# Performance work log

Hardware: AMD Instinct MI355X
Metric: run time of the kernel (lower is better)

The kernel has to match this reference:

```python
import jax, jax.numpy as jnp
import numpy as np

N = 50000       # nodes
E = 800000      # edges
F_IN = 128      # dataset.num_node_features
H = 128         # hidden_channels (all equal), pool_dim
FC1, FC2 = 512, 256
G = 512         # number of graphs
C = 32          # dataset.num_classes
EPS = 1e-5      # BatchNorm eps


def setup_inputs() -> dict:
    key = jax.random.key(0)
    ks = jax.random.split(key, 16)
    rn = lambda k, s: jax.random.normal(k, s, jnp.float32) * 0.05
    return {
        "x": jax.random.normal(ks[0], (N, F_IN), jnp.float32),
        "edge_index": jax.random.randint(ks[1], (2, E), 0, N),
        "batch": jnp.sort(jax.random.randint(ks[2], (N,), 0, G)),
        "W1": rn(ks[3], (F_IN, H)), "b1": jnp.zeros((H,), jnp.float32),
        "W2": rn(ks[4], (H, H)),    "b2": jnp.zeros((H,), jnp.float32),
        "W3": rn(ks[5], (H, H)),    "b3": jnp.zeros((H,), jnp.float32),
        "W4": rn(ks[6], (H, H)),    "b4": jnp.zeros((H,), jnp.float32),
        "lw1": rn(ks[7], (H, FC1)),   "lb1": jnp.zeros((FC1,), jnp.float32),
        "lw2": rn(ks[8], (FC1, FC2)), "lb2": jnp.zeros((FC2,), jnp.float32),
        "lw3": rn(ks[9], (FC2, C)),   "lb3": jnp.zeros((C,), jnp.float32),
        "g1": jnp.ones((FC1,), jnp.float32), "be1": jnp.zeros((FC1,), jnp.float32),
        "g2": jnp.ones((FC2,), jnp.float32), "be2": jnp.zeros((FC2,), jnp.float32),
    }


def _gcn_structure(edge_index):
    # add self loops, then symmetric deg^-1/2 normalization (PyG GCNConv default)
    loop = jnp.arange(N)
    src = jnp.concatenate([edge_index[0], loop])
    dst = jnp.concatenate([edge_index[1], loop])
    deg = jax.ops.segment_sum(jnp.ones_like(src, jnp.float32), dst, num_segments=N)
    dinv = jnp.where(deg > 0, jax.lax.rsqrt(deg), 0.0)
    norm = dinv[src] * dinv[dst]          # [E + N]
    return src, dst, norm


def _gcn_conv(x, src, dst, norm, W, b):
    h = x @ W                              # [N, out]
    agg = jax.ops.segment_sum(h[src] * norm[:, None], dst, num_segments=N)
    return agg + b


def _bn(h, gamma, beta):
    # training-mode batch stats (biased variance), as torch BatchNorm1d
    m = jnp.mean(h, axis=0)
    v = jnp.var(h, axis=0)
    return (h - m) * jax.lax.rsqrt(v + EPS) * gamma + beta


def reference(x, edge_index, batch, W1, b1, W2, b2, W3, b3, W4, b4,
              lw1, lb1, lw2, lb2, lw3, lb3, g1, be1, g2, be2):
    src, dst, norm = _gcn_structure(edge_index)
    x = jax.nn.relu(_gcn_conv(x, src, dst, norm, W1, b1))
    x = jax.nn.relu(_gcn_conv(x, src, dst, norm, W2, b2))
    x = jax.nn.relu(_gcn_conv(x, src, dst, norm, W3, b3))
    x = jax.nn.relu(_gcn_conv(x, src, dst, norm, W4, b4))
    # global_add_pool over graphs
    p = jax.ops.segment_sum(x, batch, num_segments=G)   # [G, H]
    h = jax.nn.relu(p @ lw1 + lb1)
    h = _bn(h, g1, be1)                                  # dropout = identity (eval)
    h = jax.nn.relu(h @ lw2 + lb2)
    h = _bn(h, g2, be2)
    return jax.nn.sigmoid(h @ lw3 + lb3)                 # [G, C]
```

## Files before the change

kernel.cpp:

```cpp
#include <hip/hip_runtime.h>
#include <hip/hip_fp16.h>
#include <math.h>

#define NN 50000
#define NE 800000
#define FT 128
#define NG 512
#define F1 512
#define F2 256
#define NC 32
#define BN_EPS 1e-5f

typedef __attribute__((ext_vector_type(8))) unsigned short ushort8;
typedef __attribute__((ext_vector_type(8))) _Float16 f16x8;
typedef __attribute__((ext_vector_type(4))) float f32x4;

__device__ __forceinline__ unsigned short f2h(float f) {
  return __half_as_ushort(__float2half(f));
}
__device__ __forceinline__ float h2f(unsigned short h) {
  return __half2float(__ushort_as_half(h));
}


__global__ __launch_bounds__(256) void k_hist(const int* __restrict__ ei, int* __restrict__ cnt,
                                              unsigned short* __restrict__ rank16) {
  int e = blockIdx.x * 256 + threadIdx.x;
  if (e < NE) rank16[e] = (unsigned short)atomicAdd(&cnt[ei[NE + e]], 1);
}

__global__ __launch_bounds__(256) void k_dinv(const int* __restrict__ cnt, float* __restrict__ dinv) {
  int i = blockIdx.x * 256 + threadIdx.x;
  if (i < NN) dinv[i] = rsqrtf((float)(cnt[i] + 1));
}

__global__ __launch_bounds__(256) void k_scan1(const int* __restrict__ cnt, int* __restrict__ bsum) {
  __shared__ int s[256];
  int t = threadIdx.x, i = blockIdx.x * 256 + t;
  s[t] = (i < NN) ? cnt[i] : 0;
  __syncthreads();
  for (int d = 128; d > 0; d >>= 1) {
    if (t < d) s[t] += s[t + d];
    __syncthreads();
  }
  if (t == 0) bsum[blockIdx.x] = s[0];
}

__global__ __launch_bounds__(256) void k_scan2(const int* __restrict__ bsum, int* __restrict__ bscan, int nb) {
  __shared__ int s[256];
  int t = threadIdx.x;
  int v = (t < nb) ? bsum[t] : 0;
  s[t] = v; __syncthreads();
  for (int d = 1; d < 256; d <<= 1) {
    int a = (t >= d) ? s[t - d] : 0;
    __syncthreads();
    s[t] += a;
    __syncthreads();
  }
  bscan[t] = s[t] - v;
}

__global__ __launch_bounds__(256) void k_scan3(const int* __restrict__ cnt, const int* __restrict__ bscan,
                                               int* __restrict__ off) {
  __shared__ int s[256];
  int t = threadIdx.x, i = blockIdx.x * 256 + t;
  int v = (i < NN) ? cnt[i] : 0;
  s[t] = v; __syncthreads();
  for (int d = 1; d < 256; d <<= 1) {
    int a = (t >= d) ? s[t - d] : 0;
    __syncthreads();
    s[t] += a;
    __syncthreads();
  }
  int base = bscan[blockIdx.x];
  if (i < NN) off[i] = base + s[t] - v;
  if (i == NN - 1) off[NN] = base + s[t];
}

__global__ __launch_bounds__(256) void k_fill(const int* __restrict__ ei, const int* __restrict__ off,
                                              const unsigned short* __restrict__ rank16,
                                              const float* __restrict__ dinv,
                                              unsigned int* __restrict__ ep) {
  int e = blockIdx.x * 256 + threadIdx.x;
  if (e >= NE) return;
  int s = ei[e], d = ei[NE + e];
  int p = off[d] + (int)rank16[e];
  float w = dinv[s] * dinv[d];
  ep[p] = (unsigned int)(s & 0xFFFF) | ((unsigned int)f2h(w) << 16);
}


__global__ __launch_bounds__(256) void k_wprep4(const float* __restrict__ W0, const float* __restrict__ W1,
                                                const float* __restrict__ W2, const float* __restrict__ W3,
                                                unsigned short* __restrict__ Wt) {
  int idx = blockIdx.x * 256 + threadIdx.x;
  int l = idx >> 14;
  int r = idx & 16383;
  int c = r >> 7, k = r & 127;
  const float* W = (l == 0) ? W0 : (l == 1) ? W1 : (l == 2) ? W2 : W3;
  int byte = c * 256 + k * 2;
  byte ^= (c & 7) << 4;
  Wt[l * 16384 + (byte >> 1)] = f2h(W[k * FT + c]);
}


template <int FIRST>
__global__ __launch_bounds__(256) void k_gemm_mfma(const float* __restrict__ Xf,
                                                   const unsigned short* __restrict__ Xh,
                                                   const unsigned short* __restrict__ Wt,
                                                   unsigned short* __restrict__ Oc) {
  __shared__ unsigned short sA[64 * 128];
  __shared__ unsigned short sB[128 * 128];
  int t = threadIdx.x;
#pragma unroll
  for (int i = 0; i < 8; ++i) {
    int off = t * 16 + i * 4096;
    *(float4*)((char*)sB + off) = *(const float4*)((const char*)Wt + off);
  }
  {
    int row = t >> 2, k0 = (t & 3) * 32;
    int grow = blockIdx.x * 64 + row;
    if (grow >= NN) grow = NN - 1;
    if (FIRST) {
      const float* xr = Xf + (size_t)grow * FT + k0;
#pragma unroll
      for (int j = 0; j < 4; ++j) {
        float4 v0 = *(const float4*)&xr[j * 8];
        float4 v1 = *(const float4*)&xr[j * 8 + 4];
        ushort8 w;
        w[0] = f2h(v0.x); w[1] = f2h(v0.y); w[2] = f2h(v0.z); w[3] = f2h(v0.w);
        w[4] = f2h(v1.x); w[5] = f2h(v1.y); w[6] = f2h(v1.z); w[7] = f2h(v1.w);
        int byte = row * 256 + (k0 + j * 8) * 2;
        byte ^= (row & 7) << 4;
        *(ushort8*)((char*)sA + byte) = w;
      }
    } else {
#pragma unroll
      for (int j = 0; j < 4; ++j) {
        int k = k0 + j * 8;
        int ch = k >> 5, ko = k & 31;
        ushort8 v = *(const ushort8*)&Xh[((size_t)ch * NN + grow) * 32 + ko];
        int byte = row * 256 + k * 2;
        byte ^= (row & 7) << 4;
        *(ushort8*)((char*)sA + byte) = v;
      }
    }
  }
  __syncthreads();
  int w = t >> 6, l = t & 63;
  int m = l & 15, ks = l >> 4;
  f16x8 a[4];
#pragma unroll
  for (int kk = 0; kk < 4; ++kk) {
    int r = w * 16 + m;
    int byte = r * 256 + (kk * 32 + ks * 8) * 2;
    byte ^= (r & 7) << 4;
    a[kk] = *(const f16x8*)((const char*)sA + byte);
  }
  f32x4 acc[8];
#pragma unroll
  for (int nf = 0; nf < 8; ++nf) acc[nf] = (f32x4){0.f, 0.f, 0.f, 0.f};
#pragma unroll
  for (int nf = 0; nf < 8; ++nf) {
#pragma unroll
    for (int kk = 0; kk < 4; ++kk) {
      int col = nf * 16 + m;
      int byte = col * 256 + (kk * 32 + ks * 8) * 2;
      byte ^= (col & 7) << 4;
      f16x8 b = *(const f16x8*)((const char*)sB + byte);
      acc[nf] = __builtin_amdgcn_mfma_f32_16x16x32_f16(a[kk], b, acc[nf], 0, 0, 0);
    }
  }
  int orow0 = blockIdx.x * 64 + w * 16 + ks * 4;
#pragma unroll
  for (int nf = 0; nf < 8; ++nf) {
    int ch = nf >> 1;
    int co = ((nf & 1) << 4) + m;
#pragma unroll
    for (int r = 0; r < 4; ++r) {
      int orow = orow0 + r;
      if (orow < NN) Oc[((size_t)ch * NN + orow) * 32 + co] = f2h(acc[nf][r]);
    }
  }
}


__global__ __launch_bounds__(256) void k_aggc(const unsigned short* __restrict__ Hc,
                                              const float* __restrict__ dinv,
                                              const int* __restrict__ off, const unsigned int* __restrict__ ep,
                                              const float* __restrict__ bias, unsigned short* __restrict__ O) {
  int c = blockIdx.x & 3;
  int grp = blockIdx.x >> 2;
  int t = threadIdx.x;
  int node = grp * 64 + (t >> 2);
  int l = t & 3;
  if (node >= NN) return;
  const unsigned short* base = Hc + (size_t)c * NN * 32 + l * 8;
  float di = dinv[node];
  float sw = di * di;
  float acc[8];
  {
    ushort8 sv = *(const ushort8*)&base[(size_t)node * 32];
#pragma unroll
    for (int i = 0; i < 8; ++i) acc[i] = h2f(sv[i]) * sw;
  }
  int e0 = off[node], e1 = off[node + 1];
  int e = e0;
  for (; e + 8 <= e1; e += 8) {
    unsigned int pw[8];
#pragma unroll
    for (int j = 0; j < 8; ++j) pw[j] = ep[e + j];
    ushort8 v[8];
#pragma unroll
    for (int j = 0; j < 8; ++j) v[j] = *(const ushort8*)&base[(size_t)(pw[j] & 0xFFFFu) * 32];
#pragma unroll
    for (int j = 0; j < 8; ++j) {
      float w = h2f((unsigned short)(pw[j] >> 16));
#pragma unroll
      for (int i = 0; i < 8; ++i) acc[i] += h2f(v[j][i]) * w;
    }
  }
  for (; e + 4 <= e1; e += 4) {
    unsigned int p0 = ep[e], p1 = ep[e + 1], p2 = ep[e + 2], p3 = ep[e + 3];
    ushort8 v0 = *(const ushort8*)&base[(size_t)(p0 & 0xFFFFu) * 32];
    ushort8 v1 = *(const ushort8*)&base[(size_t)(p1 & 0xFFFFu) * 32];
    ushort8 v2 = *(const ushort8*)&base[(size_t)(p2 & 0xFFFFu) * 32];
    ushort8 v3 = *(const ushort8*)&base[(size_t)(p3 & 0xFFFFu) * 32];
    float w0 = h2f((unsigned short)(p0 >> 16));
    float w1 = h2f((unsigned short)(p1 >> 16));
    float w2 = h2f((unsigned short)(p2 >> 16));
    float w3 = h2f((unsigned short)(p3 >> 16));
#pragma unroll
    for (int i = 0; i < 8; ++i) acc[i] += h2f(v0[i]) * w0;
#pragma unroll
    for (int i = 0; i < 8; ++i) acc[i] += h2f(v1[i]) * w1;
#pragma unroll
    for (int i = 0; i < 8; ++i) acc[i] += h2f(v2[i]) * w2;
#pragma unroll
    for (int i = 0; i < 8; ++i) acc[i] += h2f(v3[i]) * w3;
  }
  for (; e < e1; ++e) {
    unsigned int pv = ep[e];
    float w = h2f((unsigned short)(pv >> 16));
    ushort8 v = *(const ushort8*)&base[(size_t)(pv & 0xFFFFu) * 32];
#pragma unroll
    for (int i = 0; i < 8; ++i) acc[i] += h2f(v[i]) * w;
  }
  ushort8 outv;
#pragma unroll
  for (int i = 0; i < 8; ++i) {
    float v = acc[i] + bias[c * 32 + l * 8 + i];
    outv[i] = f2h(fmaxf(v, 0.f));
  }
  *(ushort8*)&O[((size_t)c * NN + node) * 32 + l * 8] = outv;
}


__global__ __launch_bounds__(256) void k_bounds(const int* __restrict__ batch, int* __restrict__ gstart,
                                                int* __restrict__ gend) {
  int i = blockIdx.x * 256 + threadIdx.x;
  if (i >= NN) return;
  int b = batch[i];
  if (i == 0 || batch[i - 1] != b) gstart[b] = i;
  if (i == NN - 1 || batch[i + 1] != b) gend[b] = i + 1;
}

__global__ __launch_bounds__(128) void k_pool(const unsigned short* __restrict__ X, const int* __restrict__ gstart,
                                              const int* __restrict__ gend, float* __restrict__ pool) {
  int g = blockIdx.x, t = threadIdx.x;
  int ch = t >> 5, wo = t & 31;
  float s = 0.f;
  int n0 = gstart[g], n1 = gend[g];
  const unsigned short* base = X + (size_t)ch * NN * 32 + wo;
  for (int n = n0; n < n1; ++n) s += h2f(base[(size_t)n * 32]);
  pool[g * FT + t] = s;
}


__global__ __launch_bounds__(256) void k_fc1(const float* __restrict__ P, const float* __restrict__ W,
                                             const float* __restrict__ B, float* __restrict__ O) {
  __shared__ float sp[FT];
  int g = blockIdx.x, t = threadIdx.x;
  if (t < FT) sp[t] = P[g * FT + t];
  __syncthreads();
  float a0 = B[t], a1 = B[t + 256];
  for (int k = 0; k < FT; ++k) {
    float x = sp[k];
    a0 += x * W[k * F1 + t];
    a1 += x * W[k * F1 + t + 256];
  }
  O[g * F1 + t] = fmaxf(a0, 0.f);
  O[g * F1 + t + 256] = fmaxf(a1, 0.f);
}

__global__ __launch_bounds__(256) void k_bnstats(const float* __restrict__ h, int cols,
                                                 float* __restrict__ bm, float* __restrict__ br) {
  __shared__ float ss[256], s2[256];
  int c = blockIdx.x, t = threadIdx.x;
  float a = 0.f, b = 0.f;
  for (int r = t; r < NG; r += 256) {
    float v = h[r * cols + c];
    a += v; b += v * v;
  }
  ss[t] = a; s2[t] = b; __syncthreads();
  for (int d = 128; d > 0; d >>= 1) {
    if (t < d) { ss[t] += ss[t + d]; s2[t] += s2[t + d]; }
    __syncthreads();
  }
  if (t == 0) {
    float m = ss[0] / NG;
    float var = s2[0] / NG - m * m;
    bm[c] = m;
    br[c] = rsqrtf(var + BN_EPS);
  }
}

__global__ __launch_bounds__(256) void k_fc2(const float* __restrict__ H1, const float* __restrict__ bm,
                                             const float* __restrict__ br, const float* __restrict__ gam,
                                             const float* __restrict__ bet, const float* __restrict__ W,
                                             const float* __restrict__ B, float* __restrict__ O) {
  __shared__ float sh[F1];
  int g = blockIdx.x, t = threadIdx.x;
  for (int k = t; k < F1; k += 256) {
    float v = H1[g * F1 + k];
    sh[k] = (v - bm[k]) * br[k] * gam[k] + bet[k];
  }
  __syncthreads();
  float a = B[t];
  for (int k = 0; k < F1; ++k) a += sh[k] * W[k * F2 + t];
  O[g * F2 + t] = fmaxf(a, 0.f);
}

__global__ __launch_bounds__(256) void k_fc3(const float* __restrict__ H2, const float* __restrict__ bm,
                                             const float* __restrict__ br, const float* __restrict__ gam,
                                             const float* __restrict__ bet, const float* __restrict__ W,
                                             const float* __restrict__ B, float* __restrict__ O) {
  __shared__ float sh[F2];
  int g = blockIdx.x, t = threadIdx.x;
  if (t < F2) {
    float v = H2[g * F2 + t];
    sh[t] = (v - bm[t]) * br[t] * gam[t] + bet[t];
  }
  __syncthreads();
  if (t < NC) {
    float a = B[t];
    for (int k = 0; k < F2; ++k) a += sh[k] * W[k * NC + t];
    O[g * NC + t] = 1.f / (1.f + expf(-a));
  }
}


extern "C" void kernel_launch(void* const* d_in, const int* in_sizes, int n_in,
                              void* d_out, int out_size, void* d_ws, size_t ws_size,
                              hipStream_t stream) {
  const float* x     = (const float*)d_in[0];
  const int*   ei    = (const int*)d_in[1];
  const int*   batch = (const int*)d_in[2];
  const float* Wc[4] = {(const float*)d_in[3], (const float*)d_in[5], (const float*)d_in[7], (const float*)d_in[9]};
  const float* Bc[4] = {(const float*)d_in[4], (const float*)d_in[6], (const float*)d_in[8], (const float*)d_in[10]};
  const float* lw1 = (const float*)d_in[11]; const float* lb1 = (const float*)d_in[12];
  const float* lw2 = (const float*)d_in[13]; const float* lb2 = (const float*)d_in[14];
  const float* lw3 = (const float*)d_in[15]; const float* lb3 = (const float*)d_in[16];
  const float* g1  = (const float*)d_in[17]; const float* be1 = (const float*)d_in[18];
  const float* g2  = (const float*)d_in[19]; const float* be2 = (const float*)d_in[20];

  char* p = (char*)d_ws;
  auto take = [&](size_t bytes) {
    char* r = p;
    p += (bytes + 255) & ~(size_t)255;
    return r;
  };
  int*   cnt    = (int*)take((size_t)NN * 4);
  float* dinv   = (float*)take((size_t)NN * 4);
  int*   off    = (int*)take((size_t)(NN + 1) * 4);
  int*   bsum   = (int*)take(256 * 4);
  int*   bscan  = (int*)take(256 * 4);
  int*   gstart = (int*)take((size_t)NG * 4);
  int*   gend   = (int*)take((size_t)NG * 4);
  unsigned short* rank16 = (unsigned short*)take((size_t)NE * 2);
  unsigned int*   ep   = (unsigned int*)take((size_t)NE * 4);
  unsigned short* Wt   = (unsigned short*)take((size_t)4 * FT * FT * 2);
  unsigned short* bufT = (unsigned short*)take((size_t)NN * FT * 2);
  unsigned short* bufA = (unsigned short*)take((size_t)NN * FT * 2);
  unsigned short* bufB = (unsigned short*)take((size_t)NN * FT * 2);
  float* pool   = (float*)take((size_t)NG * FT * 4);
  float* h1     = (float*)take((size_t)NG * F1 * 4);
  float* h2     = (float*)take((size_t)NG * F2 * 4);
  float* bnm1   = (float*)take(F1 * 4);
  float* bnr1   = (float*)take(F1 * 4);
  float* bnm2   = (float*)take(F2 * 4);
  float* bnr2   = (float*)take(F2 * 4);

  const int NB = (NN + 255) / 256;

  hipMemsetAsync(cnt, 0, (size_t)NN * 4, stream);
  hipMemsetAsync(gstart, 0, (size_t)NG * 4, stream);
  hipMemsetAsync(gend, 0, (size_t)NG * 4, stream);

  k_hist<<<NE / 256, 256, 0, stream>>>(ei, cnt, rank16);
  k_dinv<<<NB, 256, 0, stream>>>(cnt, dinv);
  k_scan1<<<NB, 256, 0, stream>>>(cnt, bsum);
  k_scan2<<<1, 256, 0, stream>>>(bsum, bscan, NB);
  k_scan3<<<NB, 256, 0, stream>>>(cnt, bscan, off);
  k_fill<<<NE / 256, 256, 0, stream>>>(ei, off, rank16, dinv, ep);
  k_wprep4<<<256, 256, 0, stream>>>(Wc[0], Wc[1], Wc[2], Wc[3], Wt);

  const int NBLK_G = (NN + 63) / 64;
  const int NGRP_A = (NN + 63) / 64;
  unsigned short* outs[4] = {bufA, bufB, bufA, bufB};
  for (int l = 0; l < 4; ++l) {
    if (l == 0)
      k_gemm_mfma<1><<<NBLK_G, 256, 0, stream>>>(x, (const unsigned short*)nullptr, Wt, bufT);
    else
      k_gemm_mfma<0><<<NBLK_G, 256, 0, stream>>>((const float*)nullptr, outs[l - 1], Wt + (size_t)l * FT * FT, bufT);
    k_aggc<<<NGRP_A * 4, 256, 0, stream>>>(bufT, dinv, off, ep, Bc[l], outs[l]);
  }

  k_bounds<<<NB, 256, 0, stream>>>(batch, gstart, gend);
  k_pool<<<NG, 128, 0, stream>>>(bufB, gstart, gend, pool);

  k_fc1<<<NG, 256, 0, stream>>>(pool, lw1, lb1, h1);
  k_bnstats<<<F1, 256, 0, stream>>>(h1, F1, bnm1, bnr1);
  k_fc2<<<NG, 256, 0, stream>>>(h1, bnm1, bnr1, g1, be1, lw2, lb2, h2);
  k_bnstats<<<F2, 256, 0, stream>>>(h2, F2, bnm2, bnr2);
  k_fc3<<<NG, 256, 0, stream>>>(h2, bnm2, bnr2, g2, be2, lw3, lb3, (float*)d_out);
}
```

Before: 314.3 us.

## Privatize degree histogram into 8 copies and slice CSR fill by destination range

The degree histogram now uses 8 private count arrays, chosen by block index, to cut atomic contention, and each thread loads 8 edges with vector reads. A new k_sum kernel turns the per-copy counts into exclusive prefixes and writes the total degrees. k_fill runs 8 blocks per edge strip, each writing only edges whose destination falls in one slice of nodes, which is meant to localise the scattered writes to ep. This adds an extra kernel, a larger memset, and 8x redundant edge reads in the fill step.

```diff
diff --git a/kernel.cpp b/kernel.cpp
--- a/kernel.cpp
+++ b/kernel.cpp
@@ -10,6 +10,8 @@
 #define F2 256
 #define NC 32
 #define BN_EPS 1e-5f
+#define NSLC (NN / 8)
+#define NSTRIP ((NE + 2047) / 2048)
 
 typedef __attribute__((ext_vector_type(8))) unsigned short ushort8;
 typedef __attribute__((ext_vector_type(8))) _Float16 f16x8;
@@ -23,10 +25,33 @@
 }
 
 
-__global__ __launch_bounds__(256) void k_hist(const int* __restrict__ ei, int* __restrict__ cnt,
+__global__ __launch_bounds__(256) void k_hist(const int* __restrict__ ei, int* __restrict__ cnt8,
                                               unsigned short* __restrict__ rank16) {
-  int e = blockIdx.x * 256 + threadIdx.x;
-  if (e < NE) rank16[e] = (unsigned short)atomicAdd(&cnt[ei[NE + e]], 1);
+  int c = blockIdx.x & 7;
+  int e0 = blockIdx.x * 2048 + threadIdx.x * 8;
+  if (e0 >= NE) return;
+  int* cn = cnt8 + (size_t)c * NN;
+  const int* dst = ei + NE;
+  int4 a = *(const int4*)&dst[e0];
+  int4 b4 = *(const int4*)&dst[e0 + 4];
+  int d[8] = {a.x, a.y, a.z, a.w, b4.x, b4.y, b4.z, b4.w};
+  ushort8 r;
+#pragma unroll
+  for (int j = 0; j < 8; ++j) r[j] = (unsigned short)atomicAdd(&cn[d[j]], 1);
+  *(ushort8*)&rank16[e0] = r;
+}
+
+__global__ __launch_bounds__(256) void k_sum(int* __restrict__ cnt8, int* __restrict__ cnt) {
+  int n = blockIdx.x * 256 + threadIdx.x;
+  if (n >= NN) return;
+  int s = 0;
+#pragma unroll
+  for (int c = 0; c < 8; ++c) {
+    int v = cnt8[(size_t)c * NN + n];
+    cnt8[(size_t)c * NN + n] = s;
+    s += v;
+  }
+  cnt[n] = s;
 }
 
 __global__ __launch_bounds__(256) void k_dinv(const int* __restrict__ cnt, float* __restrict__ dinv) {
@@ -78,15 +103,32 @@
 }
 
 __global__ __launch_bounds__(256) void k_fill(const int* __restrict__ ei, const int* __restrict__ off,
+                                              const int* __restrict__ pre8,
                                               const unsigned short* __restrict__ rank16,
                                               const float* __restrict__ dinv,
                                               unsigned int* __restrict__ ep) {
-  int e = blockIdx.x * 256 + threadIdx.x;
-  if (e >= NE) return;
-  int s = ei[e], d = ei[NE + e];
-  int p = off[d] + (int)rank16[e];
-  float w = dinv[s] * dinv[d];
-  ep[p] = (unsigned int)(s & 0xFFFF) | ((unsigned int)f2h(w) << 16);
+  int c = blockIdx.x & 7;
+  int lo = c * NSLC, hi = lo + NSLC;
+  int strip = blockIdx.x >> 3;
+  int e0 = strip * 2048 + threadIdx.x * 8;
+  if (e0 >= NE) return;
+  const int* prec = pre8 + (size_t)(strip & 7) * NN;
+  const int* dst = ei + NE;
+  int4 da = *(const int4*)&dst[e0];
+  int4 db = *(const int4*)&dst[e0 + 4];
+  int4 sa = *(const int4*)&ei[e0];
+  int4 sb = *(const int4*)&ei[e0 + 4];
+  ushort8 rr = *(const ushort8*)&rank16[e0];
+  int d[8] = {da.x, da.y, da.z, da.w, db.x, db.y, db.z, db.w};
+  int s[8] = {sa.x, sa.y, sa.z, sa.w, sb.x, sb.y, sb.z, sb.w};
+#pragma unroll
+  for (int j = 0; j < 8; ++j) {
+    if (d[j] >= lo && d[j] < hi) {
+      int p = off[d[j]] + prec[d[j]] + (int)rr[j];
+      float w = dinv[s[j]] * dinv[d[j]];
+      ep[p] = (unsigned int)(s[j] & 0xFFFF) | ((unsigned int)f2h(w) << 16);
+    }
+  }
 }
 
 
@@ -370,6 +412,7 @@
     p += (bytes + 255) & ~(size_t)255;
     return r;
   };
+  int*   cnt8   = (int*)take((size_t)8 * NN * 4);
   int*   cnt    = (int*)take((size_t)NN * 4);
   float* dinv   = (float*)take((size_t)NN * 4);
   int*   off    = (int*)take((size_t)(NN + 1) * 4);
@@ -393,16 +436,17 @@
 
   const int NB = (NN + 255) / 256;
 
-  hipMemsetAsync(cnt, 0, (size_t)NN * 4, stream);
+  hipMemsetAsync(cnt8, 0, (size_t)8 * NN * 4, stream);
   hipMemsetAsync(gstart, 0, (size_t)NG * 4, stream);
   hipMemsetAsync(gend, 0, (size_t)NG * 4, stream);
 
-  k_hist<<<NE / 256, 256, 0, stream>>>(ei, cnt, rank16);
+  k_hist<<<NSTRIP, 256, 0, stream>>>(ei, cnt8, rank16);
+  k_sum<<<NB, 256, 0, stream>>>(cnt8, cnt);
   k_dinv<<<NB, 256, 0, stream>>>(cnt, dinv);
   k_scan1<<<NB, 256, 0, stream>>>(cnt, bsum);
   k_scan2<<<1, 256, 0, stream>>>(bsum, bscan, NB);
   k_scan3<<<NB, 256, 0, stream>>>(cnt, bscan, off);
-  k_fill<<<NE / 256, 256, 0, stream>>>(ei, off, rank16, dinv, ep);
+  k_fill<<<NSTRIP * 8, 256, 0, stream>>>(ei, off, cnt8, rank16, dinv, ep);
   k_wprep4<<<256, 256, 0, stream>>>(Wc[0], Wc[1], Wc[2], Wc[3], Wt);
 
   const int NBLK_G = (NN + 63) / 64;
```

Result: no change. 314.8 us (+0.2%).
